# Kernel tuning notes

Hardware: AMD Instinct MI355X
Metric: run time of the kernel (lower is better)

Reference implementation:

```python
import jax, jax.numpy as jnp
import numpy as np

SQRT_DK = np.sqrt(512.0).astype(np.float32)


def setup_inputs() -> dict:
    key = jax.random.key(0)
    k1, k2, k3 = jax.random.split(key, 3)
    x = jax.random.normal(k1, (16, 2048, 512), dtype=jnp.float32)
    W1 = jax.random.normal(k2, (512, 10), dtype=jnp.float32) * 0.05
    W2 = jax.random.normal(k3, (10, 512), dtype=jnp.float32) * 0.05
    return {"x": x, "W1": W1, "W2": W2}


def reference(x, W1, W2):
    # x: [B, A, D]; low-rank bilinear scores: (x@W1) @ (W2@x^T) -> [B, A, A]
    B, A, D = x.shape
    left = jnp.einsum('bad,dr->bar', x, W1)          # [B, A, 10]
    right = jnp.einsum('rd,bcd->brc', W2, x)         # [B, 10, A]
    scores = jnp.einsum('bar,brc->bac', left, right)  # [B, A, A]
    attn = jax.nn.softmax(scores / SQRT_DK, axis=-1)
    out = jnp.einsum('bac,bcd->bad', attn, x)         # requires_value=True
    return out
```

## Files before the change

### kernel.cpp

```cpp
#include <hip/hip_runtime.h>
#include <cstdint>
#include <cstddef>


typedef float    f32x4 __attribute__((ext_vector_type(4)));
typedef _Float16 half8 __attribute__((ext_vector_type(8)));
typedef _Float16 half4 __attribute__((ext_vector_type(4)));
typedef _Float16 half2 __attribute__((ext_vector_type(2)));

#define B_  16
#define A_  2048
#define D_  512
#define KSCALE 0.06375872f

__device__ inline float fast_exp2(float v) {
#if __has_builtin(__builtin_amdgcn_exp2f)
    return __builtin_amdgcn_exp2f(v);
#else
    return __expf(v * 0.6931471805599453f);
#endif
}

__global__ __launch_bounds__(256) void kw_prep(const float* __restrict__ W1,
                                               const float* __restrict__ W2,
                                               _Float16* __restrict__ Wf) {
    int pi = blockIdx.x * 256 + threadIdx.x;
    int kt = pi >> 6, lane = pi & 63;
    int quad = lane >> 4, col = lane & 15;
    half8 h1, h2;
#pragma unroll
    for (int j = 0; j < 8; ++j) {
        int d = kt * 32 + quad * 8 + j;
        h1[j] = (col < 10) ? (_Float16)(W1[d * 10 + col] * KSCALE) : (_Float16)0.f;
        h2[j] = (col < 10) ? (_Float16)W2[col * 512 + d] : (_Float16)0.f;
    }
    *(half8*)(Wf + (size_t)pi * 16) = h1;
    *(half8*)(Wf + (size_t)pi * 16 + 8) = h2;
}

__global__ __launch_bounds__(256) void kt_transpose(const float* __restrict__ x,
                                                    _Float16* __restrict__ xT) {
    __shared__ float xs[128 * 64];
    int t = threadIdx.x, w = t >> 6;
    int bid = blockIdx.x;
    int b = bid >> 7, cg = (bid >> 3) & 15, dg = bid & 7;
    int c0 = cg << 7, d0 = dg << 6;
    const float* xb = x + ((size_t)(b * A_ + c0)) * D_ + d0;
#pragma unroll
    for (int it = 0; it < 8; ++it) {
        int slot = it * 256 + t;
        int c = slot >> 4, g = slot & 15;
        int gs = g ^ (c >> 3);
        const float* src = xb + (size_t)c * D_ + (gs << 2);
        float* dst = xs + (size_t)(it * 256 + w * 64) * 4;
        __builtin_amdgcn_global_load_lds((const __attribute__((address_space(1))) void*)src,
                                         (__attribute__((address_space(3))) void*)dst,
                                         16, 0, 0);
    }
    __syncthreads();
    _Float16* xTb = xT + ((size_t)b * D_ + d0) * A_ + c0;
#pragma unroll
    for (int p = 0; p < 4; ++p) {
        int dloc = p * 16 + (t >> 4);
        int c8 = (t & 15) << 3;
        int gd = dloc >> 2, e = dloc & 3;
        half8 h;
#pragma unroll
        for (int j = 0; j < 8; ++j) {
            int c = c8 + j;
            h[j] = (_Float16)xs[c * 64 + ((gd ^ (c >> 3)) << 2) + e];
        }
        *(half8*)(xTb + (size_t)dloc * A_ + c8) = h;
    }
}

__global__ __launch_bounds__(256) void kf_factors(const float* __restrict__ x,
                                                  const _Float16* __restrict__ Wf,
                                                  _Float16* __restrict__ left16,
                                                  _Float16* __restrict__ rightT16) {
    int t = threadIdx.x, lane = t & 63, w = t >> 6;
    int quad = lane >> 4, c16 = lane & 15;
    size_t arow0 = (size_t)blockIdx.x * 64 + (size_t)w * 16;
    const float* xa = x + (arow0 + c16) * D_;
    f32x4 accA = {0.f, 0.f, 0.f, 0.f}, accB = {0.f, 0.f, 0.f, 0.f};
#pragma unroll
    for (int kc = 0; kc < 16; ++kc) {
        float4 v0 = *(const float4*)(xa + kc * 32 + quad * 8);
        float4 v1 = *(const float4*)(xa + kc * 32 + quad * 8 + 4);
        half8 af;
        af[0] = (_Float16)v0.x; af[1] = (_Float16)v0.y; af[2] = (_Float16)v0.z; af[3] = (_Float16)v0.w;
        af[4] = (_Float16)v1.x; af[5] = (_Float16)v1.y; af[6] = (_Float16)v1.z; af[7] = (_Float16)v1.w;
        const half8* wf = (const half8*)(Wf + ((size_t)(kc * 64 + lane)) * 16);
        accA = __builtin_amdgcn_mfma_f32_16x16x32_f16(af, wf[0], accA, 0, 0, 0);
        accB = __builtin_amdgcn_mfma_f32_16x16x32_f16(af, wf[1], accB, 0, 0, 0);
    }
#pragma unroll
    for (int q = 0; q < 4; ++q) {
        size_t grow = arow0 + (size_t)quad * 4 + q;
        left16[grow * 16 + c16]   = (_Float16)accA[q];
        rightT16[grow * 16 + c16] = (_Float16)accB[q];
    }
}

__global__ __launch_bounds__(256, 4) void k3_attn(const _Float16* __restrict__ xT,
                                                  const _Float16* __restrict__ left16,
                                                  const _Float16* __restrict__ rightT16,
                                                  float* __restrict__ out) {
    __shared__ _Float16 XTl[2][128 * 32];
    __shared__ _Float16 Ps[2][128 * 40];
    __shared__ float rowsum[128];
    int t = threadIdx.x, lane = t & 63, w = t >> 6;
    int quad = lane >> 4, c16 = lane & 15;
    int bid = blockIdx.x;
    int combo = (bid & 7) | (((bid >> 7) & 7) << 3);
    int at = (bid >> 3) & 15;
    int b = combo >> 2, nb = combo & 3;
    int a0 = at << 7, n0 = nb << 7;
    int waveM = w & 1, waveN = w >> 1;

    half8 lf8[2];
#pragma unroll
    for (int i = 0; i < 2; ++i) {
        lf8[i] = (half8)(_Float16)0.f;
        if (quad < 2) {
            int arow = a0 + (2 * w + i) * 16 + c16;
            lf8[i] = *(const half8*)(left16 + ((size_t)(b << 11) + arow) * 16 + quad * 8);
        }
    }

    f32x4 acc[4][4];
#pragma unroll
    for (int mi = 0; mi < 4; ++mi)
#pragma unroll
        for (int ni = 0; ni < 4; ++ni) acc[mi][ni] = (f32x4){0.f, 0.f, 0.f, 0.f};
    float psum[2] = {0.f, 0.f};

    const _Float16* xTb = xT + ((size_t)b * D_ + n0) * A_;
    const _Float16* rTb = rightT16 + (size_t)(b << 11) * 16;

    int nloc0 = w * 32 + (lane >> 2);
    int kq = lane & 3;

    auto dma_tile = [&](int kt, int buf) {
        int c0 = kt << 5;
#pragma unroll
        for (int cc = 0; cc < 2; ++cc) {
            int nl = nloc0 + cc * 16;
            int kqs = kq ^ ((nl >> 1) & 3);
            const _Float16* src = xTb + (size_t)nl * A_ + c0 + kqs * 8;
            _Float16* dst = &XTl[buf][(w * 32 + cc * 16) * 32];
            __builtin_amdgcn_global_load_lds((const __attribute__((address_space(1))) void*)src,
                                             (__attribute__((address_space(3))) void*)dst,
                                             16, 0, 0);
        }
    };
    auto load_bfr = [&](int kt, half8* bfr) {
#pragma unroll
        for (int nh = 0; nh < 2; ++nh) {
            bfr[nh] = (half8)(_Float16)0.f;
            if (quad < 2) {
                int crow = (kt << 5) + nh * 16 + c16;
                bfr[nh] = *(const half8*)(rTb + (size_t)crow * 16 + quad * 8);
            }
        }
    };
    auto p_phase = [&](const half8* bfr, int buf) {
#pragma unroll
        for (int nh = 0; nh < 2; ++nh) {
#pragma unroll
            for (int i = 0; i < 2; ++i) {
                f32x4 z = {0.f, 0.f, 0.f, 0.f};
                f32x4 pc = __builtin_amdgcn_mfma_f32_16x16x32_f16(bfr[nh], lf8[i], z, 0, 0, 0);
                float e0 = fast_exp2(pc[0]), e1 = fast_exp2(pc[1]);
                float e2 = fast_exp2(pc[2]), e3 = fast_exp2(pc[3]);
                psum[i] += (e0 + e1) + (e2 + e3);
                half4 pv;
                pv[0] = (_Float16)e0; pv[1] = (_Float16)e1;
                pv[2] = (_Float16)e2; pv[3] = (_Float16)e3;
                *(half4*)&Ps[buf][((2 * w + i) * 16 + c16) * 40 + nh * 16 + quad * 4] = pv;
            }
        }
    };

    {
        half8 bfr0[2];
        dma_tile(0, 0);
        load_bfr(0, bfr0);
        p_phase(bfr0, 0);
    }

    for (int kt = 0; kt < 64; ++kt) {
        __syncthreads();
        int cb = kt & 1, nxt = kt + 1;
        half8 bfr[2];
        if (nxt < 64) {
            dma_tile(nxt, nxt & 1);
            load_bfr(nxt, bfr);
        }
        half8 bf[4];
#pragma unroll
        for (int ni = 0; ni < 4; ++ni) {
            int nr = waveN * 64 + ni * 16 + c16;
            bf[ni] = *(const half8*)&XTl[cb][nr * 32 + ((quad ^ ((nr >> 1) & 3)) << 3)];
        }
#pragma unroll
        for (int mi = 0; mi < 4; ++mi) {
            half8 af = *(const half8*)&Ps[cb][(waveM * 64 + mi * 16 + c16) * 40 + quad * 8];
#pragma unroll
            for (int ni = 0; ni < 4; ++ni)
                acc[mi][ni] = __builtin_amdgcn_mfma_f32_16x16x32_f16(af, bf[ni], acc[mi][ni], 0, 0, 0);
        }
        if (nxt < 64) p_phase(bfr, nxt & 1);
    }

#pragma unroll
    for (int i = 0; i < 2; ++i) {
        float s = psum[i];
        s += __shfl_xor(s, 16);
        s += __shfl_xor(s, 32);
        if (quad == 0) rowsum[(2 * w + i) * 16 + c16] = s;
    }
    __syncthreads();

    float* ob = out + ((size_t)b * A_ + a0) * D_ + n0;
#pragma unroll
    for (int mi = 0; mi < 4; ++mi) {
#pragma unroll
        for (int q = 0; q < 4; ++q) {
            int ar = waveM * 64 + mi * 16 + quad * 4 + q;
            float sc = 1.0f / rowsum[ar];
#pragma unroll
            for (int ni = 0; ni < 4; ++ni)
                ob[(size_t)ar * D_ + waveN * 64 + ni * 16 + c16] = acc[mi][ni][q] * sc;
        }
    }
}

extern "C" void kernel_launch(void* const* d_in, const int* in_sizes, int n_in,
                              void* d_out, int out_size, void* d_ws, size_t ws_size,
                              hipStream_t stream) {
    const float* x  = (const float*)d_in[0];
    const float* W1 = (const float*)d_in[1];
    const float* W2 = (const float*)d_in[2];
    float* out = (float*)d_out;
    char* ws = (char*)d_ws;
    _Float16* xT      = (_Float16*)ws;
    _Float16* left16  = (_Float16*)(ws + 33554432);
    _Float16* rightT16= (_Float16*)(ws + 34603008);
    _Float16* Wf      = (_Float16*)(ws + 35651584);

    kw_prep<<<4, 256, 0, stream>>>(W1, W2, Wf);
    kt_transpose<<<2048, 256, 0, stream>>>(x, xT);
    kf_factors<<<512, 256, 0, stream>>>(x, Wf, left16, rightT16);
    k3_attn<<<1024, 256, 0, stream>>>(xT, left16, rightT16, out);
}
```

Before: 215.2 us.

## Widen attention block to 256 output columns with 512 threads and raise MFMA priority

```diff
diff --git a/kernel.cpp b/kernel.cpp
--- a/kernel.cpp
+++ b/kernel.cpp
@@ -102,30 +102,26 @@
     }
 }
 
-__global__ __launch_bounds__(256, 4) void k3_attn(const _Float16* __restrict__ xT,
+__global__ __launch_bounds__(512, 4) void k3_attn(const _Float16* __restrict__ xT,
                                                   const _Float16* __restrict__ left16,
                                                   const _Float16* __restrict__ rightT16,
                                                   float* __restrict__ out) {
-    __shared__ _Float16 XTl[2][128 * 32];
+    __shared__ _Float16 XTl[2][256 * 32];
     __shared__ _Float16 Ps[2][128 * 40];
     __shared__ float rowsum[128];
     int t = threadIdx.x, lane = t & 63, w = t >> 6;
     int quad = lane >> 4, c16 = lane & 15;
     int bid = blockIdx.x;
-    int combo = (bid & 7) | (((bid >> 7) & 7) << 3);
+    int combo = (bid & 7) | (((bid >> 7) & 3) << 3);
     int at = (bid >> 3) & 15;
-    int b = combo >> 2, nb = combo & 3;
-    int a0 = at << 7, n0 = nb << 7;
+    int b = combo >> 1, nb = combo & 1;
+    int a0 = at << 7, n0 = nb << 8;
     int waveM = w & 1, waveN = w >> 1;
 
-    half8 lf8[2];
-#pragma unroll
-    for (int i = 0; i < 2; ++i) {
-        lf8[i] = (half8)(_Float16)0.f;
-        if (quad < 2) {
-            int arow = a0 + (2 * w + i) * 16 + c16;
-            lf8[i] = *(const half8*)(left16 + ((size_t)(b << 11) + arow) * 16 + quad * 8);
-        }
+    half8 lf8 = (half8)(_Float16)0.f;
+    if (quad < 2) {
+        int arow = a0 + w * 16 + c16;
+        lf8 = *(const half8*)(left16 + ((size_t)(b << 11) + arow) * 16 + quad * 8);
     }
 
     f32x4 acc[4][4];
@@ -133,7 +129,7 @@
     for (int mi = 0; mi < 4; ++mi)
 #pragma unroll
         for (int ni = 0; ni < 4; ++ni) acc[mi][ni] = (f32x4){0.f, 0.f, 0.f, 0.f};
-    float psum[2] = {0.f, 0.f};
+    float psum = 0.f;
 
     const _Float16* xTb = xT + ((size_t)b * D_ + n0) * A_;
     const _Float16* rTb = rightT16 + (size_t)(b << 11) * 16;
@@ -167,18 +163,15 @@
     auto p_phase = [&](const half8* bfr, int buf) {
 #pragma unroll
         for (int nh = 0; nh < 2; ++nh) {
-#pragma unroll
-            for (int i = 0; i < 2; ++i) {
-                f32x4 z = {0.f, 0.f, 0.f, 0.f};
-                f32x4 pc = __builtin_amdgcn_mfma_f32_16x16x32_f16(bfr[nh], lf8[i], z, 0, 0, 0);
-                float e0 = fast_exp2(pc[0]), e1 = fast_exp2(pc[1]);
-                float e2 = fast_exp2(pc[2]), e3 = fast_exp2(pc[3]);
-                psum[i] += (e0 + e1) + (e2 + e3);
-                half4 pv;
-                pv[0] = (_Float16)e0; pv[1] = (_Float16)e1;
-                pv[2] = (_Float16)e2; pv[3] = (_Float16)e3;
-                *(half4*)&Ps[buf][((2 * w + i) * 16 + c16) * 40 + nh * 16 + quad * 4] = pv;
-            }
+            f32x4 z = {0.f, 0.f, 0.f, 0.f};
+            f32x4 pc = __builtin_amdgcn_mfma_f32_16x16x32_f16(bfr[nh], lf8, z, 0, 0, 0);
+            float e0 = fast_exp2(pc[0]), e1 = fast_exp2(pc[1]);
+            float e2 = fast_exp2(pc[2]), e3 = fast_exp2(pc[3]);
+            psum += (e0 + e1) + (e2 + e3);
+            half4 pv;
+            pv[0] = (_Float16)e0; pv[1] = (_Float16)e1;
+            pv[2] = (_Float16)e2; pv[3] = (_Float16)e3;
+            *(half4*)&Ps[buf][(w * 16 + c16) * 40 + nh * 16 + quad * 4] = pv;
         }
     };
 
@@ -203,6 +196,7 @@
             int nr = waveN * 64 + ni * 16 + c16;
             bf[ni] = *(const half8*)&XTl[cb][nr * 32 + ((quad ^ ((nr >> 1) & 3)) << 3)];
         }
+        __builtin_amdgcn_s_setprio(1);
 #pragma unroll
         for (int mi = 0; mi < 4; ++mi) {
             half8 af = *(const half8*)&Ps[cb][(waveM * 64 + mi * 16 + c16) * 40 + quad * 8];
@@ -210,15 +204,15 @@
             for (int ni = 0; ni < 4; ++ni)
                 acc[mi][ni] = __builtin_amdgcn_mfma_f32_16x16x32_f16(af, bf[ni], acc[mi][ni], 0, 0, 0);
         }
+        __builtin_amdgcn_s_setprio(0);
         if (nxt < 64) p_phase(bfr, nxt & 1);
     }
 
-#pragma unroll
-    for (int i = 0; i < 2; ++i) {
-        float s = psum[i];
+    {
+        float s = psum;
         s += __shfl_xor(s, 16);
         s += __shfl_xor(s, 32);
-        if (quad == 0) rowsum[(2 * w + i) * 16 + c16] = s;
+        if (quad == 0) rowsum[w * 16 + c16] = s;
     }
     __syncthreads();
 
@@ -252,5 +246,5 @@
     kw_prep<<<4, 256, 0, stream>>>(W1, W2, Wf);
     kt_transpose<<<2048, 256, 0, stream>>>(x, xT);
     kf_factors<<<512, 256, 0, stream>>>(x, Wf, left16, rightT16);
-    k3_attn<<<1024, 256, 0, stream>>>(xT, left16, rightT16, out);
-}
+    k3_attn<<<512, 512, 0, stream>>>(xT, left16, rightT16, out);
+}
```

Measured after the change: 208.1 us. 3.3% less time.
